# Kernel tuning notes

Hardware: AMD Instinct MI355X
Metric: run time of the kernel (lower is better)

## Reference

```python
import jax, jax.numpy as jnp
import numpy as np

NUM_SINK = 8  # cfg.SINKHORN_ITERS


def _sinkhorn_log(c, log_a, log_b, lambd):
    # c: [M+1, N+1] augmented coupling scores (sinkhorn_unrolled: log_p = -c/lambd)
    log_p = -c / lambd
    for _ in range(NUM_SINK):  # fixed small unroll, matches num_sink
        log_p = log_p - (jax.nn.logsumexp(log_p, axis=-2, keepdims=True) - log_b[None, :])
        log_p = log_p - (jax.nn.logsumexp(log_p, axis=-1, keepdims=True) - log_a[:, None])
    return jnp.exp(log_p)


def setup_inputs() -> dict:
    key = jax.random.key(0)
    k1, k2 = jax.random.split(key)
    G, M, N, D = 128, 512, 512, 512
    return {
        "det_feats": jax.random.normal(k1, (G, N, D), dtype=jnp.float32),
        "tra_feats": jax.random.normal(k2, (G, M, D), dtype=jnp.float32),
        "alpha": jnp.ones((1,), dtype=jnp.float32),
        "eplison": jnp.zeros((1,), dtype=jnp.float32),
    }


def reference(det_feats, tra_feats, alpha, eplison):
    G, N, D = det_feats.shape
    M = tra_feats.shape[1]
    # cosine affinity per graph: [G, M, N]
    corr = jnp.einsum('gmd,gnd->gmn', tra_feats, det_feats)
    n1 = jnp.linalg.norm(tra_feats, axis=-1)  # [G, M]
    n2 = jnp.linalg.norm(det_feats, axis=-1)  # [G, N]
    affinity = corr / (n1[:, :, None] * n2[:, None, :])
    a = alpha[0]
    bins0 = jnp.broadcast_to(a, (G, M, 1)).astype(affinity.dtype)
    bins1 = jnp.broadcast_to(a, (G, 1, N)).astype(affinity.dtype)
    corner = jnp.broadcast_to(a, (G, 1, 1)).astype(affinity.dtype)
    couplings = jnp.concatenate([
        jnp.concatenate([affinity, bins0], axis=-1),
        jnp.concatenate([bins1, corner], axis=-1),
    ], axis=-2)  # [G, M+1, N+1]
    norm = 1.0 / (M + N)
    a_aug = jnp.full((M + 1,), norm, dtype=jnp.float32).at[-1].set(norm * N)
    b_aug = jnp.full((N + 1,), norm, dtype=jnp.float32).at[-1].set(norm * M)
    log_a = jnp.log(a_aug)
    log_b = jnp.log(b_aug)
    lambd = jnp.exp(eplison[0]) + 0.03
    pred = jax.vmap(lambda c: _sinkhorn_log(c, log_a, log_b, lambd))(couplings)
    return pred  # [G, M+1, N+1]
```

## Files before the change

kernel.cpp:

```cpp
#include <hip/hip_runtime.h>
#include <hip/hip_bf16.h>

#define G    128
#define MDIM 512
#define NDIM 512
#define DDIM 512
#define NORMC 0.0009765625f
#define BINW  0.5f
#define PW   516

using short8 = __attribute__((ext_vector_type(8))) short;
using short4v = __attribute__((ext_vector_type(4))) short;
using f32x4 = __attribute__((ext_vector_type(4))) float;

__device__ inline float bf2f(unsigned short u) {
    unsigned int x = ((unsigned int)u) << 16;
    return __builtin_bit_cast(float, x);
}
__device__ inline unsigned short f2bf(float f) {
    return __builtin_bit_cast(unsigned short, __float2bfloat16(f));
}
__device__ inline short4v cvt4(float4 f) {
    short4v r;
    r[0] = __builtin_bit_cast(short, __float2bfloat16(f.x));
    r[1] = __builtin_bit_cast(short, __float2bfloat16(f.y));
    r[2] = __builtin_bit_cast(short, __float2bfloat16(f.z));
    r[3] = __builtin_bit_cast(short, __float2bfloat16(f.w));
    return r;
}

__global__ __launch_bounds__(256)
void gt_cvt_kernel(const float* __restrict__ tra, const float* __restrict__ det,
                   unsigned short* __restrict__ trab, unsigned short* __restrict__ detb)
{
    int wave = threadIdx.x >> 6, lane = threadIdx.x & 63;
    long row = (long)blockIdx.x * 4 + wave;
    const long per = (long)G * MDIM;
    const float* src; unsigned short* dst; long r;
    if (row < per) { src = tra; dst = trab; r = row; }
    else           { src = det; dst = detb; r = row - per; }
    const float4* p = reinterpret_cast<const float4*>(src + r * DDIM);
    float4 x0 = p[lane];
    float4 x1 = p[lane + 64];
    float s = x0.x*x0.x + x0.y*x0.y + x0.z*x0.z + x0.w*x0.w
            + x1.x*x1.x + x1.y*x1.y + x1.z*x1.z + x1.w*x1.w;
    #pragma unroll
    for (int off = 1; off < 64; off <<= 1) s += __shfl_xor(s, off);
    float rs = rsqrtf(s);
    float4 y0 = make_float4(x0.x*rs, x0.y*rs, x0.z*rs, x0.w*rs);
    float4 y1 = make_float4(x1.x*rs, x1.y*rs, x1.z*rs, x1.w*rs);
    unsigned short* drow = dst + (size_t)r * 512;
    *reinterpret_cast<short4v*>(drow + lane * 4)       = cvt4(y0);
    *reinterpret_cast<short4v*>(drow + 256 + lane * 4) = cvt4(y1);
}

__global__ __launch_bounds__(256)
void gt_gemm_bf16(const unsigned short* __restrict__ trab, const unsigned short* __restrict__ detb,
                  const float* __restrict__ eps,
                  unsigned short* __restrict__ Ke, float* __restrict__ P1)
{
    __shared__ short As[128 * 40];
    __shared__ short Bs[128 * 40];
    int bid = blockIdx.x;
    int xcd = bid & 7, slot = bid >> 3;
    int g = xcd * 16 + (slot >> 4);
    int tile = slot & 15;
    int tm = tile >> 2, tn = tile & 3;
    int t = threadIdx.x, lane = t & 63, wave = t >> 6;
    int wr = wave >> 1, wc = wave & 1;
    f32x4 acc[4][4] = {};
    const unsigned short* Ab = trab + ((size_t)g << 18) + (size_t)(tm * 128) * 512;
    const unsigned short* Bb = detb + ((size_t)g << 18) + (size_t)(tn * 128) * 512;
    int srow = t >> 2;
    int sslot = t & 3;

    for (int kt = 0; kt < 16; ++kt) {
        int k0 = kt * 32;
        #pragma unroll
        for (int p = 0; p < 2; ++p) {
            int row = p * 64 + srow;
            short8 a = *reinterpret_cast<const short8*>(Ab + (size_t)row * 512 + k0 + sslot * 8);
            short8 b = *reinterpret_cast<const short8*>(Bb + (size_t)row * 512 + k0 + sslot * 8);
            *reinterpret_cast<short8*>(&As[row * 40 + sslot * 8]) = a;
            *reinterpret_cast<short8*>(&Bs[row * 40 + sslot * 8]) = b;
        }
        __syncthreads();
        short8 af[4], bfv[4];
        #pragma unroll
        for (int i = 0; i < 4; ++i) {
            int arow = wr * 64 + i * 16 + (lane & 15);
            af[i]  = *reinterpret_cast<const short8*>(&As[arow * 40 + (lane >> 4) * 8]);
            int brow = wc * 64 + i * 16 + (lane & 15);
            bfv[i] = *reinterpret_cast<const short8*>(&Bs[brow * 40 + (lane >> 4) * 8]);
        }
        #pragma unroll
        for (int i = 0; i < 4; ++i)
            #pragma unroll
            for (int j = 0; j < 4; ++j)
                acc[i][j] = __builtin_amdgcn_mfma_f32_16x16x32_bf16(af[i], bfv[j], acc[i][j], 0, 0, 0);
        __syncthreads();
    }

    float lam = __expf(eps[0]) + 0.03f;
    float nscale = -1.0f / lam;
    size_t kbase = (size_t)g << 18;
    int r0v = (lane >> 4) * 4;
    int c0 = lane & 15;
    #pragma unroll
    for (int j = 0; j < 4; ++j) {
        int lcol = wc * 64 + j * 16 + c0;
        int colg = tn * 128 + lcol;
        float cacc = 0.f;
        #pragma unroll
        for (int i = 0; i < 4; ++i) {
            int lrow = wr * 64 + i * 16 + r0v;
            #pragma unroll
            for (int r = 0; r < 4; ++r) {
                float ev = __expf(acc[i][j][r] * nscale);
                cacc += ev;
                int rowg = tm * 128 + lrow + r;
                Ke[kbase + (size_t)rowg * 512 + colg] = f2bf(ev);
            }
        }
        cacc += __shfl_down(cacc, 32);
        cacc += __shfl_down(cacc, 16);
        if (lane < 16)
            P1[(size_t)g * (8 * PW) + (size_t)(2 * tm + wr) * PW + tn * 128 + wc * 64 + j * 16 + lane] = cacc;
    }
}

__global__ __launch_bounds__(256)
void gt_gemm_legacy(const float* __restrict__ tra, const float* __restrict__ det,
                    const float* __restrict__ eps,
                    float* __restrict__ Koutf, float* __restrict__ P1)
{
    __shared__ short As[128 * 40];
    __shared__ short Bs[128 * 40];
    __shared__ float rnA[128];
    __shared__ float rnB[128];
    int bid = blockIdx.x;
    int xcd = bid & 7, slot = bid >> 3;
    int g = xcd * 16 + (slot >> 4);
    int tile = slot & 15;
    int tm = tile >> 2, tn = tile & 3;
    int t = threadIdx.x, lane = t & 63, wave = t >> 6;
    int wr = wave >> 1, wc = wave & 1;
    f32x4 acc[4][4] = {};
    const float* Abase = tra + (size_t)g * MDIM * DDIM + (size_t)(tm * 128) * DDIM;
    const float* Bbase = det + (size_t)g * NDIM * DDIM + (size_t)(tn * 128) * DDIM;
    int srow = t >> 3, scol = t & 7;
    float ssA[4] = {0.f, 0.f, 0.f, 0.f};
    float ssB[4] = {0.f, 0.f, 0.f, 0.f};

    for (int kt = 0; kt < 16; ++kt) {
        int k0 = kt * 32;
        #pragma unroll
        for (int p = 0; p < 4; ++p) {
            int row = p * 32 + srow;
            float4 a = *reinterpret_cast<const float4*>(Abase + (size_t)row * DDIM + k0 + scol * 4);
            float4 b = *reinterpret_cast<const float4*>(Bbase + (size_t)row * DDIM + k0 + scol * 4);
            ssA[p] += a.x*a.x + a.y*a.y + a.z*a.z + a.w*a.w;
            ssB[p] += b.x*b.x + b.y*b.y + b.z*b.z + b.w*b.w;
            *reinterpret_cast<short4v*>(&As[row * 40 + scol * 4]) = cvt4(a);
            *reinterpret_cast<short4v*>(&Bs[row * 40 + scol * 4]) = cvt4(b);
        }
        __syncthreads();
        short8 af[4], bfv[4];
        #pragma unroll
        for (int i = 0; i < 4; ++i) {
            int arow = wr * 64 + i * 16 + (lane & 15);
            af[i]  = *reinterpret_cast<const short8*>(&As[arow * 40 + (lane >> 4) * 8]);
            int brow = wc * 64 + i * 16 + (lane & 15);
            bfv[i] = *reinterpret_cast<const short8*>(&Bs[brow * 40 + (lane >> 4) * 8]);
        }
        #pragma unroll
        for (int i = 0; i < 4; ++i)
            #pragma unroll
            for (int j = 0; j < 4; ++j)
                acc[i][j] = __builtin_amdgcn_mfma_f32_16x16x32_bf16(af[i], bfv[j], acc[i][j], 0, 0, 0);
        __syncthreads();
    }

    #pragma unroll
    for (int p = 0; p < 4; ++p) {
        float a = ssA[p], b = ssB[p];
        a += __shfl_xor(a, 1); a += __shfl_xor(a, 2); a += __shfl_xor(a, 4);
        b += __shfl_xor(b, 1); b += __shfl_xor(b, 2); b += __shfl_xor(b, 4);
        if (scol == 0) { rnA[p * 32 + srow] = rsqrtf(a); rnB[p * 32 + srow] = rsqrtf(b); }
    }
    __syncthreads();

    float lam = __expf(eps[0]) + 0.03f;
    float nscale = -1.0f / lam;
    size_t obase = (size_t)g * 263169;
    int r0v = (lane >> 4) * 4;
    int c0 = lane & 15;
    #pragma unroll
    for (int j = 0; j < 4; ++j) {
        int lcol = wc * 64 + j * 16 + c0;
        int colg = tn * 128 + lcol;
        float sc2 = nscale * rnB[lcol];
        float cacc = 0.f;
        #pragma unroll
        for (int i = 0; i < 4; ++i) {
            int lrow = wr * 64 + i * 16 + r0v;
            #pragma unroll
            for (int r = 0; r < 4; ++r) {
                float ev = __expf(acc[i][j][r] * rnA[lrow + r] * sc2);
                cacc += ev;
                int rowg = tm * 128 + lrow + r;
                Koutf[obase + (size_t)rowg * 513 + colg] = ev;
            }
        }
        cacc += __shfl_down(cacc, 32);
        cacc += __shfl_down(cacc, 16);
        if (lane < 16)
            P1[(size_t)g * (8 * PW) + (size_t)(2 * tm + wr) * PW + tn * 128 + wc * 64 + j * 16 + lane] = cacc;
    }
}

template<bool BF16>
__global__ __launch_bounds__(256)
void gt_iter(const void* __restrict__ Kv,
             const float* __restrict__ alpha, const float* __restrict__ eps,
             const float* __restrict__ Pread, float* __restrict__ Pwrite,
             float* __restrict__ auOut, int first, int writeP)
{
    __shared__ float bv_s[512];
    __shared__ float colpart[4][512];
    __shared__ float rtmp[4];
    __shared__ float scal[1];
    int g = blockIdx.y, rb = blockIdx.x;
    int t = threadIdx.x, lane = t & 63, wv = t >> 6;
    float lam = __expf(eps[0]) + 0.03f;
    float val = __expf(-alpha[0] / lam);
    const float* Pg = Pread + (size_t)g * (8 * PW);
    float au512p = first ? 1.0f : Pg[513];
    float cs0 = 0.f, cs1 = 0.f;
    #pragma unroll
    for (int b = 0; b < 8; ++b) { cs0 += Pg[b * PW + t]; cs1 += Pg[b * PW + t + 256]; }
    float bv0 = NORMC / (cs0 + val * au512p);
    float bv1 = NORMC / (cs1 + val * au512p);
    bv_s[t] = bv0; bv_s[t + 256] = bv1;
    float sb = bv0 + bv1;
    #pragma unroll
    for (int off = 1; off < 64; off <<= 1) sb += __shfl_xor(sb, off);
    if (lane == 0) rtmp[wv] = sb;
    __syncthreads();
    if (t == 0) {
        float S_bv = rtmp[0] + rtmp[1] + rtmp[2] + rtmp[3];
        float S_au_prev;
        if (first) S_au_prev = 513.f;
        else { float s = 0.f; for (int b = 0; b < 8; ++b) s += Pg[b * PW + 512]; S_au_prev = s + au512p; }
        float bv512 = BINW / (val * S_au_prev);
        float au512n = BINW / (val * (S_bv + bv512));
        scal[0] = bv512;
        if (rb == 0) Pwrite[(size_t)g * (8 * PW) + 513] = au512n;
    }
    __syncthreads();
    float bv512 = scal[0];

    float bvr[8];
    #pragma unroll
    for (int k = 0; k < 8; ++k) bvr[k] = bv_s[lane * 8 + k];
    float colacc[8] = {};
    float suma = 0.f;
    const size_t RS = BF16 ? 512 : 513;
    size_t base = BF16 ? ((size_t)g << 18) : ((size_t)g * 263169);
    int rowbase = rb * 64;
    for (int rr = wv; rr < 64; rr += 4) {
        int r = rowbase + rr;
        float kv[8];
        if constexpr (BF16) {
            short8 x = *reinterpret_cast<const short8*>((const unsigned short*)Kv + base + (size_t)r * RS + lane * 8);
            #pragma unroll
            for (int k = 0; k < 8; ++k) kv[k] = bf2f((unsigned short)x[k]);
        } else {
            const float* p = (const float*)Kv + base + (size_t)r * RS + lane * 8;
            #pragma unroll
            for (int k = 0; k < 8; ++k) kv[k] = p[k];
        }
        float dot = 0.f;
        #pragma unroll
        for (int k = 0; k < 8; ++k) dot += kv[k] * bvr[k];
        #pragma unroll
        for (int off = 1; off < 64; off <<= 1) dot += __shfl_xor(dot, off);
        float au_r = NORMC / (dot + val * bv512);
        suma += au_r;
        #pragma unroll
        for (int k = 0; k < 8; ++k) colacc[k] += kv[k] * au_r;
        if (lane == 0) auOut[g * 512 + r] = au_r;
    }
    if (writeP) {
        #pragma unroll
        for (int k = 0; k < 8; ++k) colpart[wv][lane * 8 + k] = colacc[k];
        if (lane == 0) rtmp[wv] = suma;
        __syncthreads();
        float s0 = colpart[0][t] + colpart[1][t] + colpart[2][t] + colpart[3][t];
        float s1 = colpart[0][t + 256] + colpart[1][t + 256] + colpart[2][t + 256] + colpart[3][t + 256];
        float* Pw = Pwrite + (size_t)g * (8 * PW) + (size_t)rb * PW;
        Pw[t] = s0; Pw[t + 256] = s1;
        if (t == 0) Pw[512] = rtmp[0] + rtmp[1] + rtmp[2] + rtmp[3];
    }
}

template<bool BF16>
__global__ __launch_bounds__(256)
void gt_final(const void* Kv, const float* __restrict__ alpha, const float* __restrict__ eps,
              const float* __restrict__ P6, const float* __restrict__ P7,
              const float* __restrict__ au, float* out)
{
    __shared__ float bv_s[512];
    __shared__ float scal[2];
    int g = blockIdx.y, rb = blockIdx.x;
    int t = threadIdx.x, lane = t & 63, wv = t >> 6;
    float lam = __expf(eps[0]) + 0.03f;
    float val = __expf(-alpha[0] / lam);
    const float* Pg = P6 + (size_t)g * (8 * PW);
    float au512_6 = Pg[513];
    float cs0 = 0.f, cs1 = 0.f;
    #pragma unroll
    for (int b = 0; b < 8; ++b) { cs0 += Pg[b * PW + t]; cs1 += Pg[b * PW + t + 256]; }
    bv_s[t] = NORMC / (cs0 + val * au512_6);
    bv_s[t + 256] = NORMC / (cs1 + val * au512_6);
    if (t == 0) {
        float s = 0.f;
        for (int b = 0; b < 8; ++b) s += Pg[b * PW + 512];
        scal[0] = BINW / (val * (s + au512_6));
        scal[1] = P7[(size_t)g * (8 * PW) + 513];
    }
    __syncthreads();
    float bv512 = scal[0], au512_7 = scal[1];
    size_t base = BF16 ? ((size_t)g << 18) : ((size_t)g * 263169);
    size_t obase = (size_t)g * 263169;
    for (int rr = wv; rr < 64; rr += 4) {
        int r = rb * 64 + rr;
        float au_r = au[g * 512 + r];
        float* orow = out + obase + (size_t)r * 513;
        if constexpr (BF16) {
            const unsigned short* kr = (const unsigned short*)Kv + base + (size_t)r * 512;
            #pragma unroll
            for (int k = 0; k < 8; ++k) {
                int j = lane + 64 * k;
                orow[j] = bf2f(kr[j]) * au_r * bv_s[j];
            }
        } else {
            const float* kr = (const float*)Kv + base + (size_t)r * 513;
            #pragma unroll
            for (int k = 0; k < 8; ++k) {
                int j = lane + 64 * k;
                orow[j] = kr[j] * au_r * bv_s[j];
            }
        }
        if (lane == 0) orow[512] = val * au_r * bv512;
    }
    if (rb == 7) {
        float* brow = out + obase + (size_t)512 * 513;
        brow[t] = val * au512_7 * bv_s[t];
        brow[t + 256] = val * au512_7 * bv_s[t + 256];
        if (t == 0) brow[512] = val * au512_7 * bv512;
    }
}

extern "C" void kernel_launch(void* const* d_in, const int* in_sizes, int n_in,
                              void* d_out, int out_size, void* d_ws, size_t ws_size,
                              hipStream_t stream) {
    const float* det   = (const float*)d_in[0];
    const float* tra   = (const float*)d_in[1];
    const float* alpha = (const float*)d_in[2];
    const float* eps   = (const float*)d_in[3];
    float* out = (float*)d_out;

    float* P0 = (float*)d_ws;
    float* P1 = P0 + (size_t)G * 8 * PW;
    float* au = P1 + (size_t)G * 8 * PW;
    unsigned short* ke = (unsigned short*)(au + (size_t)G * 512);

    size_t smallBytes = ((size_t)2 * G * 8 * PW + (size_t)G * 512) * 4;
    bool fast = ws_size >= smallBytes + ((size_t)G << 19);

    if (fast) {
        unsigned short* trab = (unsigned short*)out;
        unsigned short* detb = trab + ((size_t)G << 18);
        gt_cvt_kernel<<<(2 * G * MDIM) / 4, 256, 0, stream>>>(tra, det, trab, detb);
        gt_gemm_bf16<<<2048, 256, 0, stream>>>(trab, detb, eps, ke, P1);
        float* Pr = P1; float* Pw = P0;
        for (int it = 0; it < 8; ++it) {
            gt_iter<true><<<dim3(8, G), 256, 0, stream>>>((const void*)ke, alpha, eps, Pr, Pw, au, it == 0 ? 1 : 0, it < 7 ? 1 : 0);
            float* tmp = Pr; Pr = Pw; Pw = tmp;
        }
        gt_final<true><<<dim3(8, G), 256, 0, stream>>>((const void*)ke, alpha, eps, P0, P1, au, out);
    } else {
        gt_gemm_legacy<<<2048, 256, 0, stream>>>(tra, det, eps, out, P1);
        float* Pr = P1; float* Pw = P0;
        for (int it = 0; it < 8; ++it) {
            gt_iter<false><<<dim3(8, G), 256, 0, stream>>>((const void*)out, alpha, eps, Pr, Pw, au, it == 0 ? 1 : 0, it < 7 ? 1 : 0);
            float* tmp = Pr; Pr = Pw; Pw = tmp;
        }
        gt_final<false><<<dim3(8, G), 256, 0, stream>>>((const void*)out, alpha, eps, P0, P1, au, out);
    }
}
```

Measured before the change: 311.6 us.

## Fuse final output pass into last Sinkhorn iteration and widen conversion stores

The separate final kernel is removed. The last Sinkhorn iteration now writes the normalized transport plan straight from the K values it already holds in registers, using vector stores, instead of re-reading K and the stored row scales in an extra pass. This saves one full read of the bf16 kernel matrix and one kernel launch. The fp32-to-bf16 conversion kernel now handles two rows per wave with 16-byte stores and launches half as many blocks. In exchange, the output rows have a 513-float stride, so the 16-byte stores are not 16-byte aligned, and the per-iteration kernel is more complex through a template flag.

Result: faster. 297.5 us (-4.5%).

```diff
diff --git a/kernel.cpp b/kernel.cpp
--- a/kernel.cpp
+++ b/kernel.cpp
@@ -34,24 +34,40 @@
                    unsigned short* __restrict__ trab, unsigned short* __restrict__ detb)
 {
     int wave = threadIdx.x >> 6, lane = threadIdx.x & 63;
-    long row = (long)blockIdx.x * 4 + wave;
+    long row0 = (long)blockIdx.x * 8 + wave * 2;
     const long per = (long)G * MDIM;
-    const float* src; unsigned short* dst; long r;
-    if (row < per) { src = tra; dst = trab; r = row; }
-    else           { src = det; dst = detb; r = row - per; }
-    const float4* p = reinterpret_cast<const float4*>(src + r * DDIM);
-    float4 x0 = p[lane];
-    float4 x1 = p[lane + 64];
-    float s = x0.x*x0.x + x0.y*x0.y + x0.z*x0.z + x0.w*x0.w
-            + x1.x*x1.x + x1.y*x1.y + x1.z*x1.z + x1.w*x1.w;
-    #pragma unroll
-    for (int off = 1; off < 64; off <<= 1) s += __shfl_xor(s, off);
-    float rs = rsqrtf(s);
-    float4 y0 = make_float4(x0.x*rs, x0.y*rs, x0.z*rs, x0.w*rs);
-    float4 y1 = make_float4(x1.x*rs, x1.y*rs, x1.z*rs, x1.w*rs);
-    unsigned short* drow = dst + (size_t)r * 512;
-    *reinterpret_cast<short4v*>(drow + lane * 4)       = cvt4(y0);
-    *reinterpret_cast<short4v*>(drow + 256 + lane * 4) = cvt4(y1);
+    const float* src; unsigned short* dst; long r0;
+    if (row0 < per) { src = tra; dst = trab; r0 = row0; }
+    else            { src = det; dst = detb; r0 = row0 - per; }
+    const float4* p0 = reinterpret_cast<const float4*>(src + r0 * DDIM);
+    const float4* p1 = reinterpret_cast<const float4*>(src + (r0 + 1) * DDIM);
+    float4 a0 = p0[lane * 2], a1 = p0[lane * 2 + 1];
+    float4 b0 = p1[lane * 2], b1 = p1[lane * 2 + 1];
+    float sa = a0.x*a0.x + a0.y*a0.y + a0.z*a0.z + a0.w*a0.w
+             + a1.x*a1.x + a1.y*a1.y + a1.z*a1.z + a1.w*a1.w;
+    float sb = b0.x*b0.x + b0.y*b0.y + b0.z*b0.z + b0.w*b0.w
+             + b1.x*b1.x + b1.y*b1.y + b1.z*b1.z + b1.w*b1.w;
+    #pragma unroll
+    for (int off = 1; off < 64; off <<= 1) {
+        sa += __shfl_xor(sa, off);
+        sb += __shfl_xor(sb, off);
+    }
+    float ra = rsqrtf(sa), rb = rsqrtf(sb);
+    short8 oa, ob;
+    {
+        short4v lo = cvt4(make_float4(a0.x*ra, a0.y*ra, a0.z*ra, a0.w*ra));
+        short4v hi = cvt4(make_float4(a1.x*ra, a1.y*ra, a1.z*ra, a1.w*ra));
+        oa[0]=lo[0]; oa[1]=lo[1]; oa[2]=lo[2]; oa[3]=lo[3];
+        oa[4]=hi[0]; oa[5]=hi[1]; oa[6]=hi[2]; oa[7]=hi[3];
+    }
+    {
+        short4v lo = cvt4(make_float4(b0.x*rb, b0.y*rb, b0.z*rb, b0.w*rb));
+        short4v hi = cvt4(make_float4(b1.x*rb, b1.y*rb, b1.z*rb, b1.w*rb));
+        ob[0]=lo[0]; ob[1]=lo[1]; ob[2]=lo[2]; ob[3]=lo[3];
+        ob[4]=hi[0]; ob[5]=hi[1]; ob[6]=hi[2]; ob[7]=hi[3];
+    }
+    *reinterpret_cast<short8*>(dst + (size_t)r0 * 512 + lane * 8)       = oa;
+    *reinterpret_cast<short8*>(dst + (size_t)(r0 + 1) * 512 + lane * 8) = ob;
 }
 
 __global__ __launch_bounds__(256)
@@ -219,17 +235,18 @@
     }
 }
 
-template<bool BF16>
+template<bool BF16, bool LAST>
 __global__ __launch_bounds__(256)
 void gt_iter(const void* __restrict__ Kv,
              const float* __restrict__ alpha, const float* __restrict__ eps,
              const float* __restrict__ Pread, float* __restrict__ Pwrite,
-             float* __restrict__ auOut, int first, int writeP)
+             float* __restrict__ auOut, float* __restrict__ outp,
+             int first, int writeP)
 {
     __shared__ float bv_s[512];
     __shared__ float colpart[4][512];
     __shared__ float rtmp[4];
-    __shared__ float scal[1];
+    __shared__ float scal[2];
     int g = blockIdx.y, rb = blockIdx.x;
     int t = threadIdx.x, lane = t & 63, wv = t >> 6;
     float lam = __expf(eps[0]) + 0.03f;
@@ -255,7 +272,8 @@
         float bv512 = BINW / (val * S_au_prev);
         float au512n = BINW / (val * (S_bv + bv512));
         scal[0] = bv512;
-        if (rb == 0) Pwrite[(size_t)g * (8 * PW) + 513] = au512n;
+        scal[1] = au512n;
+        if (!LAST && rb == 0) Pwrite[(size_t)g * (8 * PW) + 513] = au512n;
     }
     __syncthreads();
     float bv512 = scal[0];
@@ -267,6 +285,7 @@
     float suma = 0.f;
     const size_t RS = BF16 ? 512 : 513;
     size_t base = BF16 ? ((size_t)g << 18) : ((size_t)g * 263169);
+    size_t obase = (size_t)g * 263169;
     int rowbase = rb * 64;
     for (int rr = wv; rr < 64; rr += 4) {
         int r = rowbase + rr;
@@ -286,12 +305,33 @@
         #pragma unroll
         for (int off = 1; off < 64; off <<= 1) dot += __shfl_xor(dot, off);
         float au_r = NORMC / (dot + val * bv512);
-        suma += au_r;
-        #pragma unroll
-        for (int k = 0; k < 8; ++k) colacc[k] += kv[k] * au_r;
-        if (lane == 0) auOut[g * 512 + r] = au_r;
-    }
-    if (writeP) {
+        if constexpr (LAST) {
+            float* orow = outp + obase + (size_t)r * 513;
+            f32x4 o0, o1;
+            #pragma unroll
+            for (int k = 0; k < 4; ++k) {
+                o0[k] = kv[k] * au_r * bvr[k];
+                o1[k] = kv[4 + k] * au_r * bvr[4 + k];
+            }
+            *reinterpret_cast<f32x4*>(orow + lane * 8)     = o0;
+            *reinterpret_cast<f32x4*>(orow + lane * 8 + 4) = o1;
+            if (lane == 0) orow[512] = val * au_r * bv512;
+        } else {
+            suma += au_r;
+            #pragma unroll
+            for (int k = 0; k < 8; ++k) colacc[k] += kv[k] * au_r;
+            if (lane == 0) auOut[g * 512 + r] = au_r;
+        }
+    }
+    if constexpr (LAST) {
+        if (rb == 7) {
+            float au512n = scal[1];
+            float* brow = outp + obase + (size_t)512 * 513;
+            brow[t] = val * au512n * bv_s[t];
+            brow[t + 256] = val * au512n * bv_s[t + 256];
+            if (t == 0) brow[512] = val * au512n * bv512;
+        }
+    } else if (writeP) {
         #pragma unroll
         for (int k = 0; k < 8; ++k) colpart[wv][lane * 8 + k] = colacc[k];
         if (lane == 0) rtmp[wv] = suma;
@@ -301,64 +341,6 @@
         float* Pw = Pwrite + (size_t)g * (8 * PW) + (size_t)rb * PW;
         Pw[t] = s0; Pw[t + 256] = s1;
         if (t == 0) Pw[512] = rtmp[0] + rtmp[1] + rtmp[2] + rtmp[3];
-    }
-}
-
-template<bool BF16>
-__global__ __launch_bounds__(256)
-void gt_final(const void* Kv, const float* __restrict__ alpha, const float* __restrict__ eps,
-              const float* __restrict__ P6, const float* __restrict__ P7,
-              const float* __restrict__ au, float* out)
-{
-    __shared__ float bv_s[512];
-    __shared__ float scal[2];
-    int g = blockIdx.y, rb = blockIdx.x;
-    int t = threadIdx.x, lane = t & 63, wv = t >> 6;
-    float lam = __expf(eps[0]) + 0.03f;
-    float val = __expf(-alpha[0] / lam);
-    const float* Pg = P6 + (size_t)g * (8 * PW);
-    float au512_6 = Pg[513];
-    float cs0 = 0.f, cs1 = 0.f;
-    #pragma unroll
-    for (int b = 0; b < 8; ++b) { cs0 += Pg[b * PW + t]; cs1 += Pg[b * PW + t + 256]; }
-    bv_s[t] = NORMC / (cs0 + val * au512_6);
-    bv_s[t + 256] = NORMC / (cs1 + val * au512_6);
-    if (t == 0) {
-        float s = 0.f;
-        for (int b = 0; b < 8; ++b) s += Pg[b * PW + 512];
-        scal[0] = BINW / (val * (s + au512_6));
-        scal[1] = P7[(size_t)g * (8 * PW) + 513];
-    }
-    __syncthreads();
-    float bv512 = scal[0], au512_7 = scal[1];
-    size_t base = BF16 ? ((size_t)g << 18) : ((size_t)g * 263169);
-    size_t obase = (size_t)g * 263169;
-    for (int rr = wv; rr < 64; rr += 4) {
-        int r = rb * 64 + rr;
-        float au_r = au[g * 512 + r];
-        float* orow = out + obase + (size_t)r * 513;
-        if constexpr (BF16) {
-            const unsigned short* kr = (const unsigned short*)Kv + base + (size_t)r * 512;
-            #pragma unroll
-            for (int k = 0; k < 8; ++k) {
-                int j = lane + 64 * k;
-                orow[j] = bf2f(kr[j]) * au_r * bv_s[j];
-            }
-        } else {
-            const float* kr = (const float*)Kv + base + (size_t)r * 513;
-            #pragma unroll
-            for (int k = 0; k < 8; ++k) {
-                int j = lane + 64 * k;
-                orow[j] = kr[j] * au_r * bv_s[j];
-            }
-        }
-        if (lane == 0) orow[512] = val * au_r * bv512;
-    }
-    if (rb == 7) {
-        float* brow = out + obase + (size_t)512 * 513;
-        brow[t] = val * au512_7 * bv_s[t];
-        brow[t + 256] = val * au512_7 * bv_s[t + 256];
-        if (t == 0) brow[512] = val * au512_7 * bv512;
     }
 }
 
@@ -382,21 +364,21 @@
     if (fast) {
         unsigned short* trab = (unsigned short*)out;
         unsigned short* detb = trab + ((size_t)G << 18);
-        gt_cvt_kernel<<<(2 * G * MDIM) / 4, 256, 0, stream>>>(tra, det, trab, detb);
+        gt_cvt_kernel<<<(2 * G * MDIM) / 8, 256, 0, stream>>>(tra, det, trab, detb);
         gt_gemm_bf16<<<2048, 256, 0, stream>>>(trab, detb, eps, ke, P1);
         float* Pr = P1; float* Pw = P0;
-        for (int it = 0; it < 8; ++it) {
-            gt_iter<true><<<dim3(8, G), 256, 0, stream>>>((const void*)ke, alpha, eps, Pr, Pw, au, it == 0 ? 1 : 0, it < 7 ? 1 : 0);
+        for (int it = 0; it < 7; ++it) {
+            gt_iter<true, false><<<dim3(8, G), 256, 0, stream>>>((const void*)ke, alpha, eps, Pr, Pw, au, nullptr, it == 0 ? 1 : 0, 1);
             float* tmp = Pr; Pr = Pw; Pw = tmp;
         }
-        gt_final<true><<<dim3(8, G), 256, 0, stream>>>((const void*)ke, alpha, eps, P0, P1, au, out);
+        gt_iter<true, true><<<dim3(8, G), 256, 0, stream>>>((const void*)ke, alpha, eps, Pr, Pw, au, out, 0, 0);
     } else {
         gt_gemm_legacy<<<2048, 256, 0, stream>>>(tra, det, eps, out, P1);
         float* Pr = P1; float* Pw = P0;
-        for (int it = 0; it < 8; ++it) {
-            gt_iter<false><<<dim3(8, G), 256, 0, stream>>>((const void*)out, alpha, eps, Pr, Pw, au, it == 0 ? 1 : 0, it < 7 ? 1 : 0);
+        for (int it = 0; it < 7; ++it) {
+            gt_iter<false, false><<<dim3(8, G), 256, 0, stream>>>((const void*)out, alpha, eps, Pr, Pw, au, nullptr, it == 0 ? 1 : 0, 1);
             float* tmp = Pr; Pr = Pw; Pw = tmp;
         }
-        gt_final<false><<<dim3(8, G), 256, 0, stream>>>((const void*)out, alpha, eps, P0, P1, au, out);
-    }
-}
+        gt_iter<false, true><<<dim3(8, G), 256, 0, stream>>>((const void*)out, alpha, eps, Pr, Pw, au, out, 0, 0);
+    }
+}
```
